# Performance work log

Measured on AMD Instinct MI355X. Metric: run time of the kernel, lower is better.

The kernel has to match this reference:

```python
import jax, jax.numpy as jnp
import numpy as np

B, S, H = 2, 2048, 1024
NH, HD = 16, 64
ROPE_BASE = 10000.0


def setup_inputs() -> dict:
    key = jax.random.key(0)
    ks = jax.random.split(key, 8)
    sc = 1.0 / np.sqrt(H)
    return {
        "hidden_states": jax.random.normal(ks[0], (B, S, H), dtype=jnp.float32),
        "position_ids": jnp.arange(S, dtype=jnp.int64 if jax.config.jax_enable_x64 else jnp.int32)[None, :],
        "Wq": jax.random.normal(ks[1], (H, H), dtype=jnp.float32) * sc,
        "bq": jax.random.normal(ks[2], (H,), dtype=jnp.float32) * 0.02,
        "Wk": jax.random.normal(ks[3], (H, H), dtype=jnp.float32) * sc,
        "bk": jax.random.normal(ks[4], (H,), dtype=jnp.float32) * 0.02,
        "Wv": jax.random.normal(ks[5], (H, H), dtype=jnp.float32) * sc,
        "bv": jax.random.normal(ks[6], (H,), dtype=jnp.float32) * 0.02,
        "Wo": jax.random.normal(ks[7], (H, H), dtype=jnp.float32) * sc,
    }


def _rotate_half(x):
    x1, x2 = x[..., : HD // 2], x[..., HD // 2:]
    return jnp.concatenate((-x2, x1), axis=-1)


def _rope_tables(seq_len, dtype):
    inv_freq = 1.0 / (ROPE_BASE ** (jnp.arange(0, HD, 2, dtype=jnp.float32) / HD))
    t = jnp.arange(seq_len, dtype=jnp.float32)
    freqs = jnp.einsum("s,d->sd", t, inv_freq)          # [S, HD/2]
    emb = jnp.concatenate((freqs, freqs), axis=-1)       # [S, HD]
    return jnp.cos(emb).astype(dtype), jnp.sin(emb).astype(dtype)


def reference(hidden_states, position_ids, Wq, bq, Wk, bk, Wv, bv, Wo):
    bsz, q_len, _ = hidden_states.shape
    # QKV projections (torch Linear: x @ W.T + b)
    q = (hidden_states @ Wq.T + bq).reshape(bsz, q_len, NH, HD).transpose(0, 2, 1, 3)
    k = (hidden_states @ Wk.T + bk).reshape(bsz, q_len, NH, HD).transpose(0, 2, 1, 3)
    v = (hidden_states @ Wv.T + bv).reshape(bsz, q_len, NH, HD).transpose(0, 2, 1, 3)
    # RoPE
    cos, sin = _rope_tables(q_len, hidden_states.dtype)
    cos = cos[position_ids][:, None]  # [1, 1, S, HD] (unsqueeze_dim=1)
    sin = sin[position_ids][:, None]
    q = q * cos + _rotate_half(q) * sin
    k = k * cos + _rotate_half(k) * sin
    # scaled dot-product attention (mask=None, dropout=0)
    scale = 1.0 / jnp.sqrt(jnp.asarray(HD, hidden_states.dtype))
    scores = jnp.einsum("bhqd,bhkd->bhqk", q, k) * scale
    probs = jax.nn.softmax(scores, axis=-1)
    attn = jnp.einsum("bhqk,bhkd->bhqd", probs, v)
    attn = attn.transpose(0, 2, 1, 3).reshape(bsz, q_len, H)
    return attn @ Wo.T
```

## Files before the change

### kernel.cpp

```cpp
#include <hip/hip_runtime.h>
#include <hip/hip_bf16.h>
#include <math.h>

#define SS 2048
#define HH 1024
#define NHH 16
#define HDD 64
#define BH 32
#define MM 4096

typedef unsigned short u16;
using bf16x8 = __attribute__((ext_vector_type(8))) short;
using floatx4 = __attribute__((ext_vector_type(4))) float;

__device__ __forceinline__ u16 f2bf(float f) {
  unsigned u = __float_as_uint(f);
  u += 0x7fffu + ((u >> 16) & 1u);
  return (u16)(u >> 16);
}
__device__ __forceinline__ unsigned pk_bf16(float a, float b) {
  union { __hip_bfloat162 h2; unsigned u; } c;
  c.h2 = __float22bfloat162_rn(float2{a, b});
  return c.u;
}
__device__ __forceinline__ unsigned pk_asm(float a, float b) {
  unsigned r;
  asm("v_cvt_pk_bf16_f32 %0, %1, %2" : "=v"(r) : "v"(a), "v"(b));
  return r;
}
__device__ __forceinline__ void gload_lds16(const u16* g, u16* l) {
  __builtin_amdgcn_global_load_lds(
      (const __attribute__((address_space(1))) void*)g,
      (__attribute__((address_space(3))) void*)l, 16, 0, 0);
}

__global__ __launch_bounds__(256) void convert_bf(
    const float* __restrict__ hs, const float* __restrict__ wq,
    const float* __restrict__ wk, const float* __restrict__ wv,
    const float* __restrict__ wo, const int* __restrict__ pos,
    u16* __restrict__ hs_b, u16* __restrict__ wq_b, u16* __restrict__ wk_b,
    u16* __restrict__ wv_b, u16* __restrict__ wo_b,
    float2* __restrict__ tab) {
  int g = blockIdx.x * 256 + threadIdx.x;
  if (g < 2097152) {
    const float* src;
    u16* dst;
    int off;
    if (g < 1048576) {
      src = hs; dst = hs_b; off = g;
    } else {
      int t = g - 1048576;
      int w = t >> 18;
      off = t & 262143;
      src = (w == 0) ? wq : (w == 1) ? wk : (w == 2) ? wv : wo;
      dst = (w == 0) ? wq_b : (w == 1) ? wk_b : (w == 2) ? wv_b : wo_b;
    }
    float4 v = ((const float4*)src)[off];
    ushort4 o = make_ushort4(f2bf(v.x), f2bf(v.y), f2bf(v.z), f2bf(v.w));
    ((ushort4*)dst)[off] = o;
  } else {
    int idx = g - 2097152;
    int s = idx >> 5, j = idx & 31;
    float p = (float)pos[s];
    const float c0 = 13.287712379549449f / 32.0f;
    float f = p * exp2f(-(float)j * c0);
    float sn, cs;
    sincosf(f, &sn, &cs);
    tab[idx] = float2{cs, sn};
  }
}

__global__ __launch_bounds__(512, 2) void mfma_gemm_qkv(
    const u16* __restrict__ X, const u16* __restrict__ W0,
    const u16* __restrict__ W1, const u16* __restrict__ W2,
    const float* __restrict__ b0, const float* __restrict__ b1,
    const float* __restrict__ b2, const float2* __restrict__ tab,
    u16* __restrict__ O0, u16* __restrict__ O1, u16* __restrict__ O2) {
  __shared__ __align__(16) u16 lds[65536];
  const int tid = threadIdx.x;
  const int lane = tid & 63;
  const int wv = __builtin_amdgcn_readfirstlane(tid >> 6);
  const int l15 = lane & 15, quad = lane >> 4;
  const int sw7 = l15 & 7;
  const int wm = wv >> 2, wn = wv & 3;
  const int r8 = lane >> 3, c7 = lane & 7;

  int wg = blockIdx.x;
  int swz = (wg & 7) * 24 + (wg >> 3);
  int bx = swz % 12, by = swz / 12;
  const int m0 = by * 256;
  const int n0g = bx * 256;
  const int wsel = n0g >> 10;
  const int n0 = n0g & 1023;
  const u16* Wsel = (wsel == 1) ? W1 : (wsel == 2) ? W2 : W0;
  const float* bsel = (wsel == 1) ? b1 : (wsel == 2) ? b2 : b0;
  u16* Osel = (wsel == 1) ? O1 : (wsel == 2) ? O2 : O0;

  u16* const ldsA = lds;
  u16* const ldsB = lds + 32768;

  const int csw = (c7 ^ r8) * 8;
  const int rA0 = (wv >> 2) * 128 + (wv & 3) * 16;
  const int rB0 = (wv >> 1) * 64 + (wv & 1) * 16;
  const u16* gA0a = X + (size_t)(m0 + rA0 + r8) * HH + csw;
  const u16* gA0b = gA0a + 8 * HH;
  const u16* gA2a = gA0a + 64 * HH;
  const u16* gA2b = gA0a + 72 * HH;
  const u16* gB0a = Wsel + (size_t)(n0 + rB0 + r8) * HH + csw;
  const u16* gB0b = gB0a + 8 * HH;
  const u16* gB1a = gB0a + 32 * HH;
  const u16* gB1b = gB0a + 40 * HH;
  const int dA0 = rA0 * 64;
  const int dA2 = dA0 + 4096;
  const int dB0 = rB0 * 64;
  const int dB1 = dB0 + 2048;

#define STAGEU(pa, pb, base, doff, buf)                  \
  do {                                                   \
    u16* d_ = (base) + (buf) * 16384 + (doff);           \
    gload_lds16((pa), d_);                               \
    gload_lds16((pb), d_ + 512);                         \
  } while (0)

  floatx4 acc[8][4];
#pragma unroll
  for (int i = 0; i < 8; ++i)
#pragma unroll
    for (int j = 0; j < 4; ++j) acc[i][j] = (floatx4){0.f, 0.f, 0.f, 0.f};

  STAGEU(gA0a, gA0b, ldsA, dA0, 0);
  STAGEU(gA2a, gA2b, ldsA, dA2, 0);
  STAGEU(gB0a, gB0b, ldsB, dB0, 0);
  STAGEU(gB1a, gB1b, ldsB, dB1, 0);
  STAGEU(gA0a + 64, gA0b + 64, ldsA, dA0, 1);
  STAGEU(gB0a + 64, gB0b + 64, ldsB, dB0, 1);
  STAGEU(gA2a + 64, gA2b + 64, ldsA, dA2, 1);
  asm volatile("s_waitcnt vmcnt(6)" ::: "memory");
  __builtin_amdgcn_s_barrier();

  const u16 *pUB1a = gB1a + 64, *pUB1b = gB1b + 64;
  const u16 *pUA0a = gA0a + 128, *pUA0b = gA0b + 128;
  const u16 *pUB0a = gB0a + 128, *pUB0b = gB0b + 128;
  const u16 *pUA2a = gA2a + 128, *pUA2b = gA2b + 128;

  bf16x8 af[4][2], bf0[2][2], bf1[2][2];

#define LOADA(Ab, hm)                                                     \
  _Pragma("unroll") for (int mb = 0; mb < 4; ++mb) {                      \
    const u16* rp_ = (Ab) + (wm * 128 + (hm) * 64 + mb * 16 + l15) * 64;  \
    af[mb][0] = *(const bf16x8*)&rp_[((quad ^ sw7) * 8)];                 \
    af[mb][1] = *(const bf16x8*)&rp_[(((4 + quad) ^ sw7) * 8)];           \
  }
#define LOADB(dst, Bb, hn)                                                \
  _Pragma("unroll") for (int nq = 0; nq < 2; ++nq) {                      \
    const u16* rp_ = (Bb) + (wn * 64 + (hn) * 32 + nq * 16 + l15) * 64;   \
    dst[nq][0] = *(const bf16x8*)&rp_[((quad ^ sw7) * 8)];                \
    dst[nq][1] = *(const bf16x8*)&rp_[(((4 + quad) ^ sw7) * 8)];          \
  }
#define MFMAQ(bfh, hm, hn)                                                \
  _Pragma("unroll") for (int mb = 0; mb < 4; ++mb)                        \
  _Pragma("unroll") for (int nq = 0; nq < 2; ++nq) {                      \
    acc[(hm) * 4 + mb][(hn) * 2 + nq] =                                   \
        __builtin_amdgcn_mfma_f32_16x16x32_bf16(                          \
            af[mb][0], bfh[nq][0], acc[(hm) * 4 + mb][(hn) * 2 + nq], 0,  \
            0, 0);                                                        \
    acc[(hm) * 4 + mb][(hn) * 2 + nq] =                                   \
        __builtin_amdgcn_mfma_f32_16x16x32_bf16(                          \
            af[mb][1], bfh[nq][1], acc[(hm) * 4 + mb][(hn) * 2 + nq], 0,  \
            0, 0);                                                        \
  }

#pragma unroll 2
  for (int t = 0; t < 16; ++t) {
    const u16* Ac = ldsA + (t & 1) * 16384;
    const u16* Bc = ldsB + (t & 1) * 16384;
    const int nb1 = (t + 1) & 1;
    const int nb2 = t & 1;
    LOADA(Ac, 0);
    LOADB(bf0, Bc, 0);
    if (t < 15) {
      STAGEU(pUB1a, pUB1b, ldsB, dB1, nb1);
      pUB1a += 64; pUB1b += 64;
    }
    __builtin_amdgcn_s_barrier();
    asm volatile("s_waitcnt lgkmcnt(0)" ::: "memory");
    __builtin_amdgcn_s_setprio(1);
    MFMAQ(bf0, 0, 0);
    __builtin_amdgcn_s_setprio(0);
    __builtin_amdgcn_s_barrier();
    LOADB(bf1, Bc, 1);
    if (t < 14) {
      STAGEU(pUA0a, pUA0b, ldsA, dA0, nb2);
      pUA0a += 64; pUA0b += 64;
    }
    __builtin_amdgcn_s_barrier();
    asm volatile("s_waitcnt lgkmcnt(0)" ::: "memory");
    __builtin_amdgcn_s_setprio(1);
    MFMAQ(bf1, 0, 1);
    __builtin_amdgcn_s_setprio(0);
    __builtin_amdgcn_s_barrier();
    LOADA(Ac, 1);
    if (t < 14) {
      STAGEU(pUB0a, pUB0b, ldsB, dB0, nb2);
      pUB0a += 64; pUB0b += 64;
    }
    __builtin_amdgcn_s_barrier();
    asm volatile("s_waitcnt lgkmcnt(0)" ::: "memory");
    __builtin_amdgcn_s_setprio(1);
    MFMAQ(bf0, 1, 0);
    __builtin_amdgcn_s_setprio(0);
    __builtin_amdgcn_s_barrier();
    if (t < 14) {
      STAGEU(pUA2a, pUA2b, ldsA, dA2, nb2);
      pUA2a += 64; pUA2b += 64;
    }
    __builtin_amdgcn_s_setprio(1);
    MFMAQ(bf1, 1, 1);
    __builtin_amdgcn_s_setprio(0);
    if (t < 14) {
      asm volatile("s_waitcnt vmcnt(6)" ::: "memory");
      __builtin_amdgcn_s_barrier();
    } else if (t == 14) {
      asm volatile("s_waitcnt vmcnt(0)" ::: "memory");
      __builtin_amdgcn_s_barrier();
    }
  }
#undef STAGEU
#undef LOADA
#undef LOADB
#undef MFMAQ

  if (wsel < 2) {
    const float qs = (wsel == 0) ? 0.125f * 1.44269504088896f : 1.0f;
    const int colb = n0 + wn * 64;
    const int h = colb >> 6;
    const float bias0 = bsel[colb + l15];
    const float bias1 = bsel[colb + 16 + l15];
    const float bias2 = bsel[colb + 32 + l15];
    const float bias3 = bsel[colb + 48 + l15];
#pragma unroll
    for (int mb = 0; mb < 8; ++mb)
#pragma unroll
      for (int r = 0; r < 4; ++r) {
        int m = m0 + wm * 128 + mb * 16 + quad * 4 + r;
        int b = m >> 11, s = m & (SS - 1);
        float2 t0 = tab[s * 32 + l15];
        float2 t1 = tab[s * 32 + 16 + l15];
        size_t obase = ((size_t)(b * NHH + h) * SS + s) * HDD;
        float x1 = acc[mb][0][r] + bias0;
        float x2 = acc[mb][2][r] + bias2;
        Osel[obase + l15] = f2bf((x1 * t0.x - x2 * t0.y) * qs);
        Osel[obase + 32 + l15] = f2bf((x2 * t0.x + x1 * t0.y) * qs);
        float y1 = acc[mb][1][r] + bias1;
        float y2 = acc[mb][3][r] + bias3;
        Osel[obase + 16 + l15] = f2bf((y1 * t1.x - y2 * t1.y) * qs);
        Osel[obase + 48 + l15] = f2bf((y2 * t1.x + y1 * t1.y) * qs);
      }
  } else {
#pragma unroll
    for (int nb = 0; nb < 4; ++nb) {
      int col = n0 + wn * 64 + nb * 16 + l15;
      int h = col >> 6, d = col & 63;
      float bias = bsel[col];
#pragma unroll
      for (int mb = 0; mb < 8; ++mb) {
        int m = m0 + wm * 128 + mb * 16 + quad * 4;
        int b = m >> 11, s = m & (SS - 1);
        uint2 w2;
        w2.x = pk_bf16(acc[mb][nb][0] + bias, acc[mb][nb][1] + bias);
        w2.y = pk_bf16(acc[mb][nb][2] + bias, acc[mb][nb][3] + bias);
        *(uint2*)&Osel[((size_t)((b * NHH + h) * HDD + d)) * SS + s] = w2;
      }
    }
  }
}

__global__ __launch_bounds__(256) void gemm_out(const u16* __restrict__ X,
                                                const u16* __restrict__ W,
                                                float* __restrict__ Ofp) {
  __shared__ __align__(16) u16 As[128 * 32];
  __shared__ __align__(16) u16 Bs[64 * 32];
  const int tid = threadIdx.x;
  const int lane = tid & 63;
  const int wvu = __builtin_amdgcn_readfirstlane(tid >> 6);
  const int l15 = lane & 15;
  const int quad = lane >> 4;
  const int wm = wvu >> 1, wn = wvu & 1;
  const int m0 = blockIdx.y * 128;
  const int n0 = blockIdx.x * 64;
  const int lr = lane >> 2;
  const int lc = lane & 3;

  floatx4 acc[4][2];
#pragma unroll
  for (int i = 0; i < 4; ++i)
#pragma unroll
    for (int j = 0; j < 2; ++j) acc[i][j] = (floatx4){0.f, 0.f, 0.f, 0.f};

  const int scol = (lc ^ ((lr >> 1) & 3)) * 8;
  const int fsw = ((l15 >> 1) & 3);

  for (int k0 = 0; k0 < HH; k0 += 32) {
#pragma unroll
    for (int u = 0; u < 2; ++u) {
      int r = u * 64 + wvu * 16 + lr;
      gload_lds16(&X[(size_t)(m0 + r) * HH + k0 + scol],
                  &As[(u * 64 + wvu * 16) * 32]);
    }
    gload_lds16(&W[(size_t)(n0 + wvu * 16 + lr) * HH + k0 + scol],
                &Bs[(wvu * 16) * 32]);
    __syncthreads();
    bf16x8 af[4], bfr[2];
#pragma unroll
    for (int mb = 0; mb < 4; ++mb)
      af[mb] = *(const bf16x8*)&As[(wm * 64 + mb * 16 + l15) * 32 +
                                   ((quad ^ fsw) * 8)];
#pragma unroll
    for (int nb = 0; nb < 2; ++nb)
      bfr[nb] = *(const bf16x8*)&Bs[(wn * 32 + nb * 16 + l15) * 32 +
                                    ((quad ^ fsw) * 8)];
#pragma unroll
    for (int mb = 0; mb < 4; ++mb)
#pragma unroll
      for (int nb = 0; nb < 2; ++nb)
        acc[mb][nb] = __builtin_amdgcn_mfma_f32_16x16x32_bf16(
            af[mb], bfr[nb], acc[mb][nb], 0, 0, 0);
    __syncthreads();
  }

#pragma unroll
  for (int mb = 0; mb < 4; ++mb)
#pragma unroll
    for (int r = 0; r < 4; ++r) {
      int m = m0 + wm * 64 + mb * 16 + quad * 4 + r;
#pragma unroll
      for (int nb = 0; nb < 2; ++nb)
        Ofp[(size_t)m * HH + n0 + wn * 32 + nb * 16 + l15] = acc[mb][nb][r];
    }
}

__global__ __launch_bounds__(256, 4) void attn_mfma(const u16* __restrict__ Qg,
                                                    const u16* __restrict__ Kg,
                                                    const u16* __restrict__ Vtg,
                                                    u16* __restrict__ A) {
  __shared__ __align__(16) u16 smem[16384];
  u16* const Ks0 = smem;
  u16* const Ks1 = smem + 4096;
  u16* const Vs0 = smem + 8192;
  u16* const Vs1 = smem + 12288;
  float* const lpart = (float*)smem;
  float* const Opart = (float*)smem + 128;

  const int tid = threadIdx.x;
  const int lane = tid & 63;
  const int wv = __builtin_amdgcn_readfirstlane(tid >> 6);
  const int l15 = lane & 15, quad = lane >> 4;
  const int sw7 = l15 & 7;
  const int bh = blockIdx.x, qt = blockIdx.y;
  const size_t hb = (size_t)bh * SS * HDD;
  const int kh = wv >> 1;
  const int qh = wv & 1;

  const int r8 = lane >> 3, c7 = lane & 7;
  const int cs = (c7 ^ r8) * 8;
  const u16* const Kt = Kg + hb;
  const u16* const Vt = Vtg + hb;
  const int row0 = (wv * 2 + 0) * 8 + r8;
  const int row1 = (wv * 2 + 1) * 8 + r8;
  const int koff0 = row0 * HDD + cs;
  const int koff1 = row1 * HDD + cs;
  const int voff0 = row0 * SS + cs;
  const int voff1 = row1 * SS + cs;
  u16* const kd0 = smem + (wv * 2 + 0) * 512;
  u16* const kd1 = smem + (wv * 2 + 1) * 512;

  gload_lds16(Qg + hb + qt * 4096 + koff0, kd0 + 4096);
  gload_lds16(Qg + hb + qt * 4096 + koff1, kd1 + 4096);
  gload_lds16(Kt + koff0, kd0);
  gload_lds16(Kt + koff1, kd1);
  gload_lds16(Vt + voff0, kd0 + 8192);
  gload_lds16(Vt + voff1, kd1 + 8192);
  __syncthreads();

  bf16x8 qf[2][2];
#pragma unroll
  for (int nb = 0; nb < 2; ++nb)
#pragma unroll
    for (int h2 = 0; h2 < 2; ++h2)
      qf[nb][h2] = *(const bf16x8*)&Ks1[(qh * 32 + nb * 16 + l15) * 64 +
                                        (((h2 * 4 + quad) ^ sw7) * 8)];
  __syncthreads();

  float l_acc[2] = {0.f, 0.f};
  floatx4 o[4][2];
#pragma unroll
  for (int dmb = 0; dmb < 4; ++dmb)
#pragma unroll
    for (int nb = 0; nb < 2; ++nb) o[dmb][nb] = (floatx4){0.f, 0.f, 0.f, 0.f};

  auto tile_compute = [&](const u16* ks, const u16* vs) {
    floatx4 st[2][2];
    __builtin_amdgcn_s_setprio(1);
#pragma unroll
    for (int kmb = 0; kmb < 2; ++kmb) {
      int krow = kh * 32 + kmb * 16 + l15;
      bf16x8 ak0 = *(const bf16x8*)&ks[krow * 64 + ((quad ^ sw7) * 8)];
      bf16x8 ak1 = *(const bf16x8*)&ks[krow * 64 + (((4 + quad) ^ sw7) * 8)];
#pragma unroll
      for (int nb = 0; nb < 2; ++nb) {
        floatx4 z = (floatx4){0.f, 0.f, 0.f, 0.f};
        z = __builtin_amdgcn_mfma_f32_16x16x32_bf16(ak0, qf[nb][0], z, 0, 0, 0);
        z = __builtin_amdgcn_mfma_f32_16x16x32_bf16(ak1, qf[nb][1], z, 0, 0, 0);
        st[kmb][nb] = z;
      }
    }
    __builtin_amdgcn_s_setprio(0);

    bf16x8 bp[2];
#pragma unroll
    for (int nb = 0; nb < 2; ++nb) {
      float p00 = __builtin_amdgcn_exp2f(st[0][nb][0]);
      float p01 = __builtin_amdgcn_exp2f(st[0][nb][1]);
      float p02 = __builtin_amdgcn_exp2f(st[0][nb][2]);
      float p03 = __builtin_amdgcn_exp2f(st[0][nb][3]);
      float p10 = __builtin_amdgcn_exp2f(st[1][nb][0]);
      float p11 = __builtin_amdgcn_exp2f(st[1][nb][1]);
      float p12 = __builtin_amdgcn_exp2f(st[1][nb][2]);
      float p13 = __builtin_amdgcn_exp2f(st[1][nb][3]);
      l_acc[nb] += ((p00 + p01) + (p02 + p03)) + ((p10 + p11) + (p12 + p13));
      union { bf16x8 v; unsigned u[4]; } pu;
      pu.u[0] = pk_asm(p00, p01);
      pu.u[1] = pk_asm(p02, p03);
      pu.u[2] = pk_asm(p10, p11);
      pu.u[3] = pk_asm(p12, p13);
      bp[nb] = pu.v;
    }

    const int cb0 = kh * 4 + (quad >> 1);
    const int cb1 = cb0 + 2;
    const int sub = (quad & 1) * 4;
    __builtin_amdgcn_s_setprio(1);
#pragma unroll
    for (int dmb = 0; dmb < 4; ++dmb) {
      int vr = (dmb * 16 + l15) * 64;
      union { bf16x8 v; uint2 d2[2]; } au;
      au.d2[0] = *(const uint2*)&vs[vr + ((cb0 ^ sw7) * 8) + sub];
      au.d2[1] = *(const uint2*)&vs[vr + ((cb1 ^ sw7) * 8) + sub];
#pragma unroll
      for (int nb = 0; nb < 2; ++nb)
        o[dmb][nb] = __builtin_amdgcn_mfma_f32_16x16x32_bf16(au.v, bp[nb],
                                                             o[dmb][nb], 0, 0, 0);
    }
    __builtin_amdgcn_s_setprio(0);
  };

  for (int tt = 0; tt < SS / 64; tt += 2) {
    {
      const int k1 = (tt + 1) * 64 * HDD;
      const int v1 = (tt + 1) * 64;
      gload_lds16(Kt + k1 + koff0, kd0 + 4096);
      gload_lds16(Kt + k1 + koff1, kd1 + 4096);
      gload_lds16(Vt + v1 + voff0, kd0 + 12288);
      gload_lds16(Vt + v1 + voff1, kd1 + 12288);
    }
    tile_compute(Ks0, Vs0);
    __syncthreads();

    if (tt < SS / 64 - 2) {
      const int k2 = (tt + 2) * 64 * HDD;
      const int v2 = (tt + 2) * 64;
      gload_lds16(Kt + k2 + koff0, kd0);
      gload_lds16(Kt + k2 + koff1, kd1);
      gload_lds16(Vt + v2 + voff0, kd0 + 8192);
      gload_lds16(Vt + v2 + voff1, kd1 + 8192);
    }
    tile_compute(Ks1, Vs1);
    __syncthreads();
  }

#pragma unroll
  for (int nb = 0; nb < 2; ++nb) {
    l_acc[nb] += __shfl_xor(l_acc[nb], 16);
    l_acc[nb] += __shfl_xor(l_acc[nb], 32);
  }
  if (quad == 0) {
    lpart[wv * 32 + l15] = l_acc[0];
    lpart[wv * 32 + 16 + l15] = l_acc[1];
  }
  if (kh == 1) {
    float* dst = Opart + qh * (32 * 68);
#pragma unroll
    for (int nb = 0; nb < 2; ++nb)
#pragma unroll
      for (int dmb = 0; dmb < 4; ++dmb)
        *(floatx4*)&dst[(nb * 16 + l15) * 68 + dmb * 16 + quad * 4] =
            o[dmb][nb];
  }
  __syncthreads();
  if (kh == 0) {
    const int b = bh >> 4, h = bh & 15;
    const float* src = Opart + qh * (32 * 68);
    float inv[2];
#pragma unroll
    for (int nb = 0; nb < 2; ++nb)
      inv[nb] = 1.f / (lpart[wv * 32 + nb * 16 + l15] +
                       lpart[(wv + 2) * 32 + nb * 16 + l15]);
#pragma unroll
    for (int nb = 0; nb < 2; ++nb) {
      int s = qt * 64 + qh * 32 + nb * 16 + l15;
#pragma unroll
      for (int dmb = 0; dmb < 4; ++dmb) {
        floatx4 part =
            *(const floatx4*)&src[(nb * 16 + l15) * 68 + dmb * 16 + quad * 4];
        floatx4 tot = (o[dmb][nb] + part) * inv[nb];
        uint2 w2;
        w2.x = pk_asm(tot[0], tot[1]);
        w2.y = pk_asm(tot[2], tot[3]);
        *(uint2*)&A[((size_t)(b * SS + s) * HH) + h * HDD + dmb * 16 +
                    quad * 4] = w2;
      }
    }
  }
}

extern "C" void kernel_launch(void* const* d_in, const int* in_sizes, int n_in,
                              void* d_out, int out_size, void* d_ws,
                              size_t ws_size, hipStream_t stream) {
  const float* hs = (const float*)d_in[0];
  const int* pos = (const int*)d_in[1];
  const float* Wq = (const float*)d_in[2];
  const float* bq = (const float*)d_in[3];
  const float* Wk = (const float*)d_in[4];
  const float* bk = (const float*)d_in[5];
  const float* Wv = (const float*)d_in[6];
  const float* bv = (const float*)d_in[7];
  const float* Wo = (const float*)d_in[8];
  float* out = (float*)d_out;

  u16* hs_b = (u16*)d_ws;
  u16* wq_b = hs_b + 4194304;
  u16* wk_b = wq_b + 1048576;
  u16* wv_b = wk_b + 1048576;
  u16* wo_b = wv_b + 1048576;
  u16* Qb = wo_b + 1048576;
  u16* Kb = Qb + 4194304;
  u16* Vtb = Kb + 4194304;
  u16* Ab = Vtb + 4194304;
  float2* tab = (float2*)(Ab + 4194304);

  hipLaunchKernelGGL(convert_bf, dim3(8448), dim3(256), 0, stream, hs, Wq, Wk,
                     Wv, Wo, pos, hs_b, wq_b, wk_b, wv_b, wo_b, tab);
  hipLaunchKernelGGL(mfma_gemm_qkv, dim3(192), dim3(512), 0, stream, hs_b,
                     wq_b, wk_b, wv_b, bq, bk, bv, tab, Qb, Kb, Vtb);
  hipLaunchKernelGGL(attn_mfma, dim3(32, 32), dim3(256), 0, stream, Qb, Kb,
                     Vtb, Ab);
  hipLaunchKernelGGL(gemm_out, dim3(16, 32), dim3(256), 0, stream, Ab, wo_b,
                     out);
}
```

Baseline: 186.3 us.

## Double-buffer output projection GEMM with larger 128x128 tiles and block swizzle

Rewrites the output-projection GEMM to use 128x128 output tiles with a K-step of 64, double-buffered in LDS. The next tile is prefetched with direct global-to-LDS loads while MFMAs run on the current one. It also adds an XOR swizzle for LDS bank conflicts, a workgroup-index remap for L2 locality, and s_setprio around the MFMA block. The goal is to hide global load latency and raise data reuse per load, at the cost of more LDS (64KB) and registers per block and fewer blocks (256).

```diff
diff --git a/kernel.cpp b/kernel.cpp
--- a/kernel.cpp
+++ b/kernel.cpp
@@ -278,55 +278,85 @@
 __global__ __launch_bounds__(256) void gemm_out(const u16* __restrict__ X,
                                                 const u16* __restrict__ W,
                                                 float* __restrict__ Ofp) {
-  __shared__ __align__(16) u16 As[128 * 32];
-  __shared__ __align__(16) u16 Bs[64 * 32];
+  __shared__ __align__(16) u16 As[2][8192];
+  __shared__ __align__(16) u16 Bs[2][8192];
   const int tid = threadIdx.x;
   const int lane = tid & 63;
-  const int wvu = __builtin_amdgcn_readfirstlane(tid >> 6);
-  const int l15 = lane & 15;
-  const int quad = lane >> 4;
-  const int wm = wvu >> 1, wn = wvu & 1;
-  const int m0 = blockIdx.y * 128;
-  const int n0 = blockIdx.x * 64;
-  const int lr = lane >> 2;
-  const int lc = lane & 3;
-
-  floatx4 acc[4][2];
+  const int wv = __builtin_amdgcn_readfirstlane(tid >> 6);
+  const int l15 = lane & 15, quad = lane >> 4;
+  const int sw7 = l15 & 7;
+  const int wm = wv >> 1, wn = wv & 1;
+  const int r8 = lane >> 3, c7 = lane & 7;
+
+  int wg = blockIdx.x;
+  int swz = (wg & 7) * 32 + (wg >> 3);
+  const int n0 = (swz & 7) * 128;
+  const int m0 = (swz >> 3) * 128;
+
+  const int csw = (c7 ^ r8) * 8;
+  const u16* gA = X + (size_t)(m0 + wv * 32 + r8) * HH + csw;
+  const u16* gB = W + (size_t)(n0 + wv * 32 + r8) * HH + csw;
+  u16* const dA = &As[0][0] + (wv * 32) * 64;
+  u16* const dB = &Bs[0][0] + (wv * 32) * 64;
+
+#define STG_O(tile, buf)                                           \
+  _Pragma("unroll") for (int u = 0; u < 4; ++u) {                  \
+    gload_lds16(gA + (size_t)u * 8 * HH + (tile) * 64,             \
+                dA + (buf) * 8192 + u * 512);                      \
+    gload_lds16(gB + (size_t)u * 8 * HH + (tile) * 64,             \
+                dB + (buf) * 8192 + u * 512);                      \
+  }
+
+  floatx4 acc[4][4];
 #pragma unroll
   for (int i = 0; i < 4; ++i)
 #pragma unroll
-    for (int j = 0; j < 2; ++j) acc[i][j] = (floatx4){0.f, 0.f, 0.f, 0.f};
-
-  const int scol = (lc ^ ((lr >> 1) & 3)) * 8;
-  const int fsw = ((l15 >> 1) & 3);
-
-  for (int k0 = 0; k0 < HH; k0 += 32) {
-#pragma unroll
-    for (int u = 0; u < 2; ++u) {
-      int r = u * 64 + wvu * 16 + lr;
-      gload_lds16(&X[(size_t)(m0 + r) * HH + k0 + scol],
-                  &As[(u * 64 + wvu * 16) * 32]);
-    }
-    gload_lds16(&W[(size_t)(n0 + wvu * 16 + lr) * HH + k0 + scol],
-                &Bs[(wvu * 16) * 32]);
-    __syncthreads();
-    bf16x8 af[4], bfr[2];
+    for (int j = 0; j < 4; ++j) acc[i][j] = (floatx4){0.f, 0.f, 0.f, 0.f};
+
+  STG_O(0, 0);
+  STG_O(1, 1);
+  asm volatile("s_waitcnt vmcnt(8)" ::: "memory");
+  __builtin_amdgcn_s_barrier();
+
+  for (int t = 0; t < 16; ++t) {
+    const u16* Ac = &As[0][0] + (t & 1) * 8192;
+    const u16* Bc = &Bs[0][0] + (t & 1) * 8192;
+    bf16x8 af[4][2], bfr[4][2];
+#pragma unroll
+    for (int mb = 0; mb < 4; ++mb) {
+      const u16* rp = Ac + (wm * 64 + mb * 16 + l15) * 64;
+      af[mb][0] = *(const bf16x8*)&rp[(quad ^ sw7) * 8];
+      af[mb][1] = *(const bf16x8*)&rp[((4 + quad) ^ sw7) * 8];
+    }
+#pragma unroll
+    for (int nb = 0; nb < 4; ++nb) {
+      const u16* rp = Bc + (wn * 64 + nb * 16 + l15) * 64;
+      bfr[nb][0] = *(const bf16x8*)&rp[(quad ^ sw7) * 8];
+      bfr[nb][1] = *(const bf16x8*)&rp[((4 + quad) ^ sw7) * 8];
+    }
+    __builtin_amdgcn_s_barrier();
+    if (t < 14) STG_O(t + 2, t & 1);
+    asm volatile("s_waitcnt lgkmcnt(0)" ::: "memory");
+    __builtin_amdgcn_sched_barrier(0);
+    __builtin_amdgcn_s_setprio(1);
 #pragma unroll
     for (int mb = 0; mb < 4; ++mb)
-      af[mb] = *(const bf16x8*)&As[(wm * 64 + mb * 16 + l15) * 32 +
-                                   ((quad ^ fsw) * 8)];
-#pragma unroll
-    for (int nb = 0; nb < 2; ++nb)
-      bfr[nb] = *(const bf16x8*)&Bs[(wn * 32 + nb * 16 + l15) * 32 +
-                                    ((quad ^ fsw) * 8)];
-#pragma unroll
-    for (int mb = 0; mb < 4; ++mb)
-#pragma unroll
-      for (int nb = 0; nb < 2; ++nb)
+#pragma unroll
+      for (int nb = 0; nb < 4; ++nb) {
         acc[mb][nb] = __builtin_amdgcn_mfma_f32_16x16x32_bf16(
-            af[mb], bfr[nb], acc[mb][nb], 0, 0, 0);
-    __syncthreads();
-  }
+            af[mb][0], bfr[nb][0], acc[mb][nb], 0, 0, 0);
+        acc[mb][nb] = __builtin_amdgcn_mfma_f32_16x16x32_bf16(
+            af[mb][1], bfr[nb][1], acc[mb][nb], 0, 0, 0);
+      }
+    __builtin_amdgcn_s_setprio(0);
+    if (t < 14) {
+      asm volatile("s_waitcnt vmcnt(8)" ::: "memory");
+    } else if (t == 14) {
+      asm volatile("s_waitcnt vmcnt(0)" ::: "memory");
+    }
+    __builtin_amdgcn_s_barrier();
+  }
+#undef STG_O
 
 #pragma unroll
   for (int mb = 0; mb < 4; ++mb)
@@ -334,8 +364,8 @@
     for (int r = 0; r < 4; ++r) {
       int m = m0 + wm * 64 + mb * 16 + quad * 4 + r;
 #pragma unroll
-      for (int nb = 0; nb < 2; ++nb)
-        Ofp[(size_t)m * HH + n0 + wn * 32 + nb * 16 + l15] = acc[mb][nb][r];
+      for (int nb = 0; nb < 4; ++nb)
+        Ofp[(size_t)m * HH + n0 + wn * 64 + nb * 16 + l15] = acc[mb][nb][r];
     }
 }
 
@@ -554,6 +584,6 @@
                      wq_b, wk_b, wv_b, bq, bk, bv, tab, Qb, Kb, Vtb);
   hipLaunchKernelGGL(attn_mfma, dim3(32, 32), dim3(256), 0, stream, Qb, Kb,
                      Vtb, Ab);
-  hipLaunchKernelGGL(gemm_out, dim3(16, 32), dim3(256), 0, stream, Ab, wo_b,
+  hipLaunchKernelGGL(gemm_out, dim3(256), dim3(256), 0, stream, Ab, wo_b,
                      out);
 }
```

Result: faster. 180.5 us, median of 2 (-3.1%).
